# Kernel optimization log

Measured on AMD Instinct MI355X. Metric: run time of the kernel, lower is better.

## Reference

```python
import jax, jax.numpy as jnp
import numpy as np
import math

D = 6       # input_size (raw particle features)
H = 128     # hidden_size
B, N, T = 128, 64, 64  # batch, objects, timesteps (T <= max_len 100)


def setup_inputs() -> dict:
    key = jax.random.key(0)
    ks = jax.random.split(key, 16)
    def lin(k, fan_in, shape):
        return (jax.random.uniform(k, shape, jnp.float32) * 2.0 - 1.0) / np.sqrt(fan_in)
    dm = D + H  # 134, PE / readout feature dim
    return {
        "x": jax.random.normal(ks[0], (B, N, T, D), jnp.float32),
        # particle_embedding Linear(D, H)
        "W_emb": lin(ks[1], D, (D, H)), "b_emb": lin(ks[2], D, (H,)),
        # GRU(H, H): torch layout (3H, in)
        "W_ih": lin(ks[3], H, (3 * H, H)), "W_hh": lin(ks[4], H, (3 * H, H)),
        "b_ih": lin(ks[5], H, (3 * H,)), "b_hh": lin(ks[6], H, (3 * H,)),
        # gate_nn: Linear(dm,H) -> SiLU -> Linear(H,1)
        "Wg1": lin(ks[7], dm, (dm, H)), "bg1": lin(ks[8], dm, (H,)),
        "Wg2": lin(ks[9], H, (H, 1)), "bg2": lin(ks[10], H, (1,)),
        # nn: Linear(dm,H) -> SiLU -> Linear(H,H)
        "Wn1": lin(ks[11], dm, (dm, H)), "bn1": lin(ks[12], dm, (H,)),
        "Wn2": lin(ks[13], H, (H, H)), "bn2": lin(ks[14], H, (H,)),
    }


def _positional_encoding(seq_len, d_model, dtype):
    pos = jnp.arange(seq_len, dtype=dtype)[:, None]                      # [T,1]
    div = jnp.exp(jnp.arange(0, d_model, 2, dtype=dtype) * (-math.log(10000.0) / d_model))
    ang = pos * div                                                       # [T, dm/2]
    # interleave sin (even idx) and cos (odd idx)
    return jnp.stack([jnp.sin(ang), jnp.cos(ang)], axis=-1).reshape(seq_len, d_model)


def _gru_last_hidden(y, W_ih, W_hh, b_ih, b_hh):
    # y: [BN, T, H]; PyTorch GRU gate order: r, z, n
    BN, Tn, Hh = y.shape
    xp = y @ W_ih.T + b_ih                       # [BN, T, 3H], input projections
    def step(h, xp_t):
        gh = h @ W_hh.T + b_hh                   # [BN, 3H]
        xr, xz, xn = jnp.split(xp_t, 3, axis=-1)
        hr, hz, hn = jnp.split(gh, 3, axis=-1)
        r = jax.nn.sigmoid(xr + hr)
        z = jax.nn.sigmoid(xz + hz)
        n = jnp.tanh(xn + r * hn)
        h_new = (1.0 - z) * n + z * h
        return h_new, None
    h0 = jnp.zeros((BN, Hh), y.dtype)
    h_last, _ = jax.lax.scan(step, h0, jnp.swapaxes(xp, 0, 1))
    return h_last                                 # [BN, H]


def reference(x, W_emb, b_emb, W_ih, W_hh, b_ih, b_hh,
              Wg1, bg1, Wg2, bg2, Wn1, bn1, Wn2, bn2):
    Bb, Nn, Tt, Dd = x.shape
    Hh = W_emb.shape[1]
    dm = Dd + Hh
    # particle embedding + GRU over time per (batch, object)
    y = (x @ W_emb + b_emb).reshape(Bb * Nn, Tt, Hh)
    h = _gru_last_hidden(y, W_ih, W_hh, b_ih, b_hh)       # [B*N, H]
    # broadcast last hidden state over timesteps, concat with raw positions
    h_exp = jnp.broadcast_to(h[:, None, :], (Bb * Nn, Tt, Hh))
    aug = jnp.concatenate([x.reshape(Bb * Nn, Tt, Dd), h_exp], axis=-1)  # [B*N, T, dm]
    aug = aug + _positional_encoding(Tt, dm, x.dtype)      # PE (dropout in eval = identity)
    feats = aug.reshape(Bb * Nn * Tt, dm)                  # [M, dm]
    # AttentionalAggregation: segment softmax over batch index
    seg = jnp.repeat(jnp.arange(Bb), Nn * Tt)              # [M]
    gate = jax.nn.silu(feats @ Wg1 + bg1) @ Wg2 + bg2      # [M, 1]
    gate = gate[:, 0]
    val = jax.nn.silu(feats @ Wn1 + bn1) @ Wn2 + bn2       # [M, H]
    gmax = jax.ops.segment_max(gate, seg, num_segments=Bb)
    e = jnp.exp(gate - gmax[seg])
    denom = jax.ops.segment_sum(e, seg, num_segments=Bb)
    w = e / denom[seg]                                      # [M]
    out = jax.ops.segment_sum(w[:, None] * val, seg, num_segments=Bb)  # [B, H]
    return out
```

## Files before the change

### kernel.cpp

```cpp
#include <hip/hip_runtime.h>

using bf8v = __bf16 __attribute__((ext_vector_type(8)));
using s4v  = short  __attribute__((ext_vector_type(4)));
using f4v  = float  __attribute__((ext_vector_type(4)));

#define L2E 1.44269504088896340f

__device__ __forceinline__ float ex2(float x){ float r; asm("v_exp_f32 %0, %1" : "=v"(r) : "v"(x)); return r; }
__device__ __forceinline__ float rcp_(float x){ float r; asm("v_rcp_f32 %0, %1" : "=v"(r) : "v"(x)); return r; }
__device__ __forceinline__ float sigm(float x){ return rcp_(1.0f + ex2(-L2E*x)); }
__device__ __forceinline__ float tanh_(float x){ return 1.0f - 2.0f*rcp_(1.0f + ex2(2.0f*L2E*x)); }
__device__ __forceinline__ short f2bf(float x){ return __builtin_bit_cast(short, (__bf16)x); }
__device__ __forceinline__ f4v splat4(float v){ f4v r = {v,v,v,v}; return r; }
__device__ __forceinline__ f4v mfma16(bf8v a, bf8v b, f4v c){
  return __builtin_amdgcn_mfma_f32_16x16x32_bf16(a, b, c, 0, 0, 0);
}

__global__ void prep_kernel(
    const float* __restrict__ x,
    const float* __restrict__ W_emb, const float* __restrict__ b_emb,
    const float* __restrict__ W_ih,  const float* __restrict__ W_hh,
    const float* __restrict__ b_ih,
    const float* __restrict__ Wg1,   const float* __restrict__ Wn1,
    const float* __restrict__ Wn2,
    const float* __restrict__ bg1,   const float* __restrict__ bn1,
    short* __restrict__ bhhf, short* __restrict__ wcf, short* __restrict__ wn2f,
    short* __restrict__ w2f, float* __restrict__ b2, float* __restrict__ pe,
    float* __restrict__ bc, short* __restrict__ xfrag)
{
  int i = blockIdx.x*256 + threadIdx.x;
  if (i < 49152){
    int e = i&7, lane=(i>>3)&63, r=i>>9; int nt=r%24, kb=r/24;
    int k = kb*32 + ((lane>>4)<<3) + e;
    int n = nt*16 + (lane&15);
    bhhf[i] = f2bf(W_hh[n*128 + k]);
    return;
  }
  i -= 49152;
  if (i < 40960){
    int e=i&7, lane=(i>>3)&63, r=i>>9; int nt=r%16, kb=r/16;
    int k = kb*32 + ((lane>>4)<<3) + e; int n = nt*16 + (lane&15);
    float v = 0.f;
    if (k < 134) v = (n < 128) ? Wg1[k*128 + n] : Wn1[k*128 + (n-128)];
    wcf[i] = f2bf(v);
    return;
  }
  i -= 40960;
  if (i < 16384){
    int e=i&7, lane=(i>>3)&63, r=i>>9; int nt=r%8, kb=r/8;
    int k = kb*32 + ((lane>>4)<<3) + e; int n = nt*16 + (lane&15);
    wn2f[i] = f2bf(Wn2[k*128 + n]);
    return;
  }
  i -= 16384;
  if (i < 12288){
    int e=i&7, lane=(i>>3)&63, nt=i>>9;
    int k = ((lane>>4)<<3) + e; int n = nt*16 + (lane&15);
    float v = 0.f;
    if (k < 6){
      const float* we = W_emb + k*128; const float* wi = W_ih + n*128;
      float s = 0.f;
      for (int h2=0; h2<128; ++h2) s += we[h2]*wi[h2];
      v = s;
    }
    w2f[i] = f2bf(v);
    return;
  }
  i -= 12288;
  if (i < 384){
    float s = b_ih[i]; const float* wi = W_ih + i*128;
    for (int h2=0; h2<128; ++h2) s += b_emb[h2]*wi[h2];
    b2[i] = s;
    return;
  }
  i -= 384;
  if (i < 10240){
    int t = i/160, k = i%160;
    float v = 0.f;
    if (k < 134){
      float fr = expf(-(float)(k & ~1) * 9.210340371976184f / 134.f);
      float a = (float)t * fr;
      v = (k&1) ? cosf(a) : sinf(a);
    }
    pe[i] = v;
    return;
  }
  i -= 10240;
  if (i < 256){ bc[i] = (i < 128) ? bg1[i] : bn1[i-128]; return; }
  i -= 256;
  if (i < 524288){
    int r = i & 15, t = (i>>4)&63, grp = i>>10;
    const float* xr = x + ((size_t)(grp*16 + r)*64 + t)*6;
    s4v lo, hi;
    lo[0]=f2bf(xr[0]); lo[1]=f2bf(xr[1]); lo[2]=f2bf(xr[2]); lo[3]=f2bf(xr[3]);
    hi[0]=f2bf(xr[4]); hi[1]=f2bf(xr[5]); hi[2]=0; hi[3]=0;
    *reinterpret_cast<s4v*>(xfrag + (size_t)i*8)     = lo;
    *reinterpret_cast<s4v*>(xfrag + (size_t)i*8 + 4) = hi;
    return;
  }
}

__global__ __launch_bounds__(512, 2) void gru_kernel(
    const short* __restrict__ xfrag,
    const short* __restrict__ bhhf,
    const short* __restrict__ w2f,
    const float* __restrict__ b2,
    const float* __restrict__ b_hh,
    float* __restrict__ h_out)
{
  __shared__ alignas(16) short h_lds[2][2][16*128];
  const int tid = threadIdx.x;
  const int w = tid >> 6;
  const int lane = tid & 63;
  const int l15 = lane & 15, lhi = lane >> 4;
  const int blk = blockIdx.x;

  for (int i = tid; i < 16*128; i += 512){ h_lds[0][0][i] = 0; h_lds[1][0][i] = 0; }

  bf8v bhh[4][3]; bf8v w2v[3];
  float b2v[3], bhv[3];
  #pragma unroll
  for (int g = 0; g < 3; ++g){
    int nt = g*8 + w;
    w2v[g] = *reinterpret_cast<const bf8v*>(w2f + ((nt*64 + lane)<<3));
    #pragma unroll
    for (int kb = 0; kb < 4; ++kb)
      bhh[kb][g] = *reinterpret_cast<const bf8v*>(bhhf + (((kb*24 + nt)*64 + lane)<<3));
    int col = nt*16 + l15;
    b2v[g] = b2[col]; bhv[g] = b_hh[col];
  }
  float hr0[4] = {0.f,0.f,0.f,0.f};
  float hr1[4] = {0.f,0.f,0.f,0.f};
  __syncthreads();

  const short* xf0 = xfrag + (size_t)(2*blk  )*8192 + l15*8;
  const short* xf1 = xfrag + (size_t)(2*blk+1)*8192 + l15*8;
  const int sw_r = (l15 & 7) << 4;

  bf8v ax0 = *reinterpret_cast<const bf8v*>(xf0);
  bf8v ax1 = *reinterpret_cast<const bf8v*>(xf1);

#define GSTEP(P, T)                                                           \
  {                                                                           \
    int tn = (T) + 1; if (tn > 63) tn = 63;                                   \
    bf8v axn0 = *reinterpret_cast<const bf8v*>(xf0 + tn*128);                 \
    bf8v axn1 = *reinterpret_cast<const bf8v*>(xf1 + tn*128);                 \
    bf8v ah0[4], ah1[4];                                                      \
    _Pragma("unroll")                                                         \
    for (int kb = 0; kb < 4; ++kb){                                           \
      int off = l15*256 + ((kb*64 + lhi*16) ^ sw_r);                          \
      ah0[kb] = *reinterpret_cast<const bf8v*>((const char*)h_lds[0][P] + off); \
      ah1[kb] = *reinterpret_cast<const bf8v*>((const char*)h_lds[1][P] + off); \
    }                                                                         \
    f4v xg0[3], gh0[3], xg1[3], gh1[3];                                       \
    _Pragma("unroll")                                                         \
    for (int g = 0; g < 3; ++g){                                              \
      xg0[g] = splat4(b2v[g]); xg0[g] = mfma16(ax0, w2v[g], xg0[g]);          \
      xg1[g] = splat4(b2v[g]); xg1[g] = mfma16(ax1, w2v[g], xg1[g]);          \
      gh0[g] = splat4(bhv[g]); gh1[g] = splat4(bhv[g]);                       \
      _Pragma("unroll")                                                       \
      for (int kb = 0; kb < 4; ++kb){                                         \
        gh0[g] = mfma16(ah0[kb], bhh[kb][g], gh0[g]);                         \
        gh1[g] = mfma16(ah1[kb], bhh[kb][g], gh1[g]);                         \
      }                                                                       \
    }                                                                         \
    _Pragma("unroll")                                                         \
    for (int r = 0; r < 4; ++r){                                              \
      int s = lhi*4 + r;                                                      \
      int woff = s*256 + (((w*16 + l15)*2) ^ ((s&7)<<4));                     \
      { float rg = sigm(xg0[0][r] + gh0[0][r]);                               \
        float zg = sigm(xg0[1][r] + gh0[1][r]);                               \
        float ng = tanh_(xg0[2][r] + rg*gh0[2][r]);                           \
        float hv = ng + zg*(hr0[r] - ng); hr0[r] = hv;                        \
        *(short*)((char*)h_lds[0][P^1] + woff) = f2bf(hv); }                  \
      { float rg = sigm(xg1[0][r] + gh1[0][r]);                               \
        float zg = sigm(xg1[1][r] + gh1[1][r]);                               \
        float ng = tanh_(xg1[2][r] + rg*gh1[2][r]);                           \
        float hv = ng + zg*(hr1[r] - ng); hr1[r] = hv;                        \
        *(short*)((char*)h_lds[1][P^1] + woff) = f2bf(hv); }                  \
    }                                                                         \
    ax0 = axn0; ax1 = axn1;                                                   \
    __syncthreads();                                                          \
  }

  for (int tt = 0; tt < 32; ++tt){
    GSTEP(0, 2*tt);
    GSTEP(1, 2*tt + 1);
  }
#undef GSTEP

  #pragma unroll
  for (int r = 0; r < 4; ++r){
    int s = lhi*4 + r;
    h_out[(size_t)((2*blk  )*16 + s)*128 + w*16 + l15] = hr0[r];
    h_out[(size_t)((2*blk+1)*16 + s)*128 + w*16 + l15] = hr1[r];
  }
}

__global__ __launch_bounds__(256, 4) void feats_kernel(
    const float* __restrict__ x, const float* __restrict__ h_out,
    const float* __restrict__ pe,
    const short* __restrict__ wcf, const short* __restrict__ wn2f,
    const float* __restrict__ bc, const float* __restrict__ Wg2,
    const float* __restrict__ bg2, const float* __restrict__ bn2,
    float* __restrict__ partials)
{
  __shared__ alignas(16) char AB[64*320];
  __shared__ alignas(16) float hb[160];
  __shared__ float gp[2][64];
  __shared__ float gate_arr[64];

  const int tid = threadIdx.x;
  const int w = tid >> 6;
  const int lane = tid & 63;
  const int l15 = lane & 15, lhi = lane >> 4;
  const int seq = blockIdx.x;

  if (tid < 160) hb[tid] = (tid >= 6 && tid < 134) ? h_out[(size_t)seq*128 + tid - 6] : 0.f;
  __syncthreads();

  {
    int m = tid >> 2, q = tid & 3, k0 = q*40;
    float xr8[8] = {0.f,0.f,0.f,0.f,0.f,0.f,0.f,0.f};
    if (q == 0){
      const float* xr = x + (size_t)(seq*64 + m)*6;
      #pragma unroll
      for (int j = 0; j < 6; ++j) xr8[j] = xr[j];
    }
    const float* per = pe + m*160 + k0;
    const f4v* hb4 = reinterpret_cast<const f4v*>(hb + k0);
    int swm = (m & 3) << 4;
    #pragma unroll
    for (int j = 0; j < 10; ++j){
      f4v v = hb4[j];
      f4v p4 = *reinterpret_cast<const f4v*>(per + 4*j);
      v += p4;
      if (j < 2){
        v[0] += xr8[4*j+0]; v[1] += xr8[4*j+1];
        v[2] += xr8[4*j+2]; v[3] += xr8[4*j+3];
      }
      s4v o;
      #pragma unroll
      for (int c = 0; c < 4; ++c) o[c] = f2bf(v[c]);
      int off = m*320 + (((k0 + 4*j)*2) ^ swm);
      *reinterpret_cast<s4v*>(AB + off) = o;
    }
  }
  __syncthreads();

  const int ntb = w*4;
  float bcv[4];
  #pragma unroll
  for (int i=0;i<4;++i) bcv[i] = bc[(ntb+i)*16 + l15];
  f4v acc[4][4];
  #pragma unroll
  for (int mt=0;mt<4;++mt)
    #pragma unroll
    for (int i=0;i<4;++i) acc[mt][i] = splat4(bcv[i]);
  #pragma unroll
  for (int kb = 0; kb < 5; ++kb){
    bf8v a[4];
    #pragma unroll
    for (int mt=0;mt<4;++mt){
      int row = l15 + 16*mt;
      int off = row*320 + ((kb*64 + lhi*16) ^ ((row&3)<<4));
      a[mt] = *reinterpret_cast<const bf8v*>(AB + off);
    }
    bf8v b[4];
    #pragma unroll
    for (int i=0;i<4;++i)
      b[i] = *reinterpret_cast<const bf8v*>(wcf + (((kb*16 + ntb + i)*64 + lane)<<3));
    #pragma unroll
    for (int mt=0;mt<4;++mt)
      #pragma unroll
      for (int i=0;i<4;++i) acc[mt][i] = mfma16(a[mt], b[i], acc[mt][i]);
  }
  __syncthreads();

  if (w < 2){
    float wg2v[4];
    #pragma unroll
    for (int i=0;i<4;++i) wg2v[i] = Wg2[(ntb+i)*16 + l15];
    #pragma unroll
    for (int mt=0;mt<4;++mt)
      #pragma unroll
      for (int r=0;r<4;++r){
        float p = 0.f;
        #pragma unroll
        for (int i=0;i<4;++i){ float v = acc[mt][i][r]; p += v*sigm(v)*wg2v[i]; }
        p += __shfl_xor(p, 1); p += __shfl_xor(p, 2);
        p += __shfl_xor(p, 4); p += __shfl_xor(p, 8);
        if (l15 == 0) gp[w][mt*16 + lhi*4 + r] = p;
      }
  } else {
    #pragma unroll
    for (int mt=0;mt<4;++mt)
      #pragma unroll
      for (int i=0;i<4;++i)
        #pragma unroll
        for (int r=0;r<4;++r){
          float v = acc[mt][i][r]; float s = v*sigm(v);
          int row = mt*16 + lhi*4 + r;
          int colb = (((w-2)*4 + i)*16 + l15)*2;
          int off = row*256 + (colb ^ ((row&7)<<4));
          *(short*)(AB + off) = f2bf(s);
        }
  }
  __syncthreads();

  if (tid < 64) gate_arr[tid] = bg2[0] + gp[0][tid] + gp[1][tid];

  const int nt2b = w*2;
  float bn2v[2];
  #pragma unroll
  for (int i=0;i<2;++i) bn2v[i] = bn2[(nt2b+i)*16 + l15];
  f4v acc2[4][2];
  #pragma unroll
  for (int mt=0;mt<4;++mt)
    #pragma unroll
    for (int i=0;i<2;++i) acc2[mt][i] = splat4(bn2v[i]);
  #pragma unroll
  for (int kb = 0; kb < 4; ++kb){
    bf8v a2f[4];
    #pragma unroll
    for (int mt=0;mt<4;++mt){
      int row = l15 + 16*mt;
      int off = row*256 + ((kb*64 + lhi*16) ^ ((row&7)<<4));
      a2f[mt] = *reinterpret_cast<const bf8v*>(AB + off);
    }
    bf8v b2f[2];
    #pragma unroll
    for (int i=0;i<2;++i)
      b2f[i] = *reinterpret_cast<const bf8v*>(wn2f + (((kb*8 + nt2b + i)*64 + lane)<<3));
    #pragma unroll
    for (int mt=0;mt<4;++mt)
      #pragma unroll
      for (int i=0;i<2;++i) acc2[mt][i] = mfma16(a2f[mt], b2f[i], acc2[mt][i]);
  }
  __syncthreads();

  float g = gate_arr[lane];
  float M = g;
  #pragma unroll
  for (int d=1; d<64; d<<=1) M = fmaxf(M, __shfl_xor(M, d));
  float e = ex2((g - M)*L2E);
  float sE = e;
  #pragma unroll
  for (int d=1; d<64; d<<=1) sE += __shfl_xor(sE, d);
  float ev0 = 0.f, ev1 = 0.f;
  #pragma unroll
  for (int mt=0;mt<4;++mt)
    #pragma unroll
    for (int r=0;r<4;++r){
      int row = mt*16 + lhi*4 + r;
      float wm = ex2((gate_arr[row] - M)*L2E);
      ev0 += wm*acc2[mt][0][r];
      ev1 += wm*acc2[mt][1][r];
    }
  ev0 += __shfl_xor(ev0, 16); ev0 += __shfl_xor(ev0, 32);
  ev1 += __shfl_xor(ev1, 16); ev1 += __shfl_xor(ev1, 32);

  float* pb = partials + (size_t)seq*130;
  if (tid == 0){ pb[0] = M; pb[1] = sE; }
  if (lane < 16){
    pb[2 + (nt2b+0)*16 + lane] = ev0;
    pb[2 + (nt2b+1)*16 + lane] = ev1;
  }
}

__global__ void combine_kernel(const float* __restrict__ partials, float* __restrict__ out)
{
  int b = blockIdx.x; int j = threadIdx.x;
  const float* pb = partials + (size_t)b*64*130;
  float M = -3.0e38f;
  for (int p = 0; p < 64; ++p) M = fmaxf(M, pb[p*130]);
  float num = 0.f, den = 0.f;
  for (int p = 0; p < 64; ++p){
    float wm = ex2((pb[p*130] - M)*L2E);
    den += wm * pb[p*130 + 1];
    num += wm * pb[p*130 + 2 + j];
  }
  out[b*128 + j] = num / den;
}

extern "C" void kernel_launch(void* const* d_in, const int* in_sizes, int n_in,
                              void* d_out, int out_size, void* d_ws, size_t ws_size,
                              hipStream_t stream) {
  (void)in_sizes; (void)n_in; (void)out_size; (void)ws_size;
  const float* x     = (const float*)d_in[0];
  const float* W_emb = (const float*)d_in[1];
  const float* b_emb = (const float*)d_in[2];
  const float* W_ih  = (const float*)d_in[3];
  const float* W_hh  = (const float*)d_in[4];
  const float* b_ih  = (const float*)d_in[5];
  const float* b_hh  = (const float*)d_in[6];
  const float* Wg1   = (const float*)d_in[7];
  const float* bg1   = (const float*)d_in[8];
  const float* Wg2   = (const float*)d_in[9];
  const float* bg2   = (const float*)d_in[10];
  const float* Wn1   = (const float*)d_in[11];
  const float* bn1   = (const float*)d_in[12];
  const float* Wn2   = (const float*)d_in[13];
  const float* bn2   = (const float*)d_in[14];

  char* p = (char*)d_ws;
  short* bhhf = (short*)p; p += 98304;
  short* wcf  = (short*)p; p += 81920;
  short* wn2f = (short*)p; p += 32768;
  short* w2f  = (short*)p; p += 24576;
  float* b2   = (float*)p; p += 1536;
  float* pe   = (float*)p; p += 40960;
  float* bc   = (float*)p; p += 1024;
  short* xfrag = (short*)p; p += (size_t)524288*8*2;
  float* h_out    = (float*)p; p += (size_t)8192*128*4;
  float* partials = (float*)p; p += (size_t)8192*130*4;

  prep_kernel<<<2555, 256, 0, stream>>>(x, W_emb, b_emb, W_ih, W_hh, b_ih,
                                        Wg1, Wn1, Wn2, bg1, bn1,
                                        bhhf, wcf, wn2f, w2f, b2, pe, bc, xfrag);
  gru_kernel<<<256, 512, 0, stream>>>(xfrag, bhhf, w2f, b2, b_hh, h_out);
  feats_kernel<<<8192, 256, 0, stream>>>(x, h_out, pe, wcf, wn2f, bc, Wg2, bg2, bn2, partials);
  combine_kernel<<<128, 128, 0, stream>>>(partials, (float*)d_out);
}
```

Measured before the change: 193.3 us.

## Factor first readout layer into per-sequence hidden term and per-timestep bias

The first-layer matmul of the gate and value MLPs is split algebraically. The hidden-state part (constant over timesteps) is computed once per sequence at the end of the GRU kernel. The positional-encoding part plus bias is precomputed as a per-timestep bias table. The feats kernel now only runs a K=32 MFMA over the raw x features, with a constant-1 column that injects the per-sequence hidden term. This removes the K=160 matmul and the LDS staging of concatenated features per block, at the cost of extra work in the GRU epilogue, bf16 rounding of the hidden contribution, and a serial 134-term loop per element in prep.

After: 256.2 us. 1.33x slower.

```diff
diff --git a/kernel.cpp b/kernel.cpp
--- a/kernel.cpp
+++ b/kernel.cpp
@@ -24,9 +24,9 @@
     const float* __restrict__ Wg1,   const float* __restrict__ Wn1,
     const float* __restrict__ Wn2,
     const float* __restrict__ bg1,   const float* __restrict__ bn1,
-    short* __restrict__ bhhf, short* __restrict__ wcf, short* __restrict__ wn2f,
-    short* __restrict__ w2f, float* __restrict__ b2, float* __restrict__ pe,
-    float* __restrict__ bc, short* __restrict__ xfrag)
+    short* __restrict__ bhhf, short* __restrict__ wcxf, short* __restrict__ wchf,
+    short* __restrict__ wn2f, short* __restrict__ w2f, float* __restrict__ b2,
+    short* __restrict__ xfrag, float* __restrict__ rowbiasT)
 {
   int i = blockIdx.x*256 + threadIdx.x;
   if (i < 49152){
@@ -37,15 +37,23 @@
     return;
   }
   i -= 49152;
-  if (i < 40960){
-    int e=i&7, lane=(i>>3)&63, r=i>>9; int nt=r%16, kb=r/16;
-    int k = kb*32 + ((lane>>4)<<3) + e; int n = nt*16 + (lane&15);
+  if (i < 8192){
+    int e=i&7, lane=(i>>3)&63, nt=i>>9;
+    int k = ((lane>>4)<<3) + e; int n = nt*16 + (lane&15);
     float v = 0.f;
-    if (k < 134) v = (n < 128) ? Wg1[k*128 + n] : Wn1[k*128 + (n-128)];
-    wcf[i] = f2bf(v);
-    return;
-  }
-  i -= 40960;
+    if (k < 6) v = (n < 128) ? Wg1[k*128 + n] : Wn1[k*128 + (n-128)];
+    wcxf[i] = f2bf(v);
+    return;
+  }
+  i -= 8192;
+  if (i < 32768){
+    int e=i&7, lane=(i>>3)&63, r=i>>9; int nt=r&15, kb=r>>4;
+    int k = 6 + kb*32 + ((lane>>4)<<3) + e; int n = nt*16 + (lane&15);
+    float v = (n < 128) ? Wg1[k*128 + n] : Wn1[k*128 + (n-128)];
+    wchf[i] = f2bf(v);
+    return;
+  }
+  i -= 32768;
   if (i < 16384){
     int e=i&7, lane=(i>>3)&63, r=i>>9; int nt=r%8, kb=r/8;
     int k = kb*32 + ((lane>>4)<<3) + e; int n = nt*16 + (lane&15);
@@ -74,28 +82,28 @@
     return;
   }
   i -= 384;
-  if (i < 10240){
-    int t = i/160, k = i%160;
-    float v = 0.f;
-    if (k < 134){
-      float fr = expf(-(float)(k & ~1) * 9.210340371976184f / 134.f);
-      float a = (float)t * fr;
-      v = (k&1) ? cosf(a) : sinf(a);
-    }
-    pe[i] = v;
-    return;
-  }
-  i -= 10240;
-  if (i < 256){ bc[i] = (i < 128) ? bg1[i] : bn1[i-128]; return; }
-  i -= 256;
   if (i < 524288){
     int r = i & 15, t = (i>>4)&63, grp = i>>10;
     const float* xr = x + ((size_t)(grp*16 + r)*64 + t)*6;
     s4v lo, hi;
     lo[0]=f2bf(xr[0]); lo[1]=f2bf(xr[1]); lo[2]=f2bf(xr[2]); lo[3]=f2bf(xr[3]);
-    hi[0]=f2bf(xr[4]); hi[1]=f2bf(xr[5]); hi[2]=0; hi[3]=0;
+    hi[0]=f2bf(xr[4]); hi[1]=f2bf(xr[5]); hi[2]=f2bf(1.0f); hi[3]=0;
     *reinterpret_cast<s4v*>(xfrag + (size_t)i*8)     = lo;
     *reinterpret_cast<s4v*>(xfrag + (size_t)i*8 + 4) = hi;
+    return;
+  }
+  i -= 524288;
+  if (i < 16384){
+    int n = i >> 6, t = i & 63;
+    float s = (n < 128) ? bg1[n] : bn1[n-128];
+    for (int k = 0; k < 134; ++k){
+      float fr = expf(-(float)(k & ~1) * 9.210340371976184f / 134.f);
+      float a = (float)t * fr;
+      float p = (k & 1) ? cosf(a) : sinf(a);
+      float wv = (n < 128) ? Wg1[k*128 + n] : Wn1[k*128 + (n-128)];
+      s += p * wv;
+    }
+    rowbiasT[i] = s;
     return;
   }
 }
@@ -106,7 +114,8 @@
     const short* __restrict__ w2f,
     const float* __restrict__ b2,
     const float* __restrict__ b_hh,
-    float* __restrict__ h_out)
+    const short* __restrict__ wchf,
+    short* __restrict__ svb)
 {
   __shared__ alignas(16) short h_lds[2][2][16*128];
   const int tid = threadIdx.x;
@@ -190,23 +199,40 @@
 #undef GSTEP
 
   #pragma unroll
-  for (int r = 0; r < 4; ++r){
-    int s = lhi*4 + r;
-    h_out[(size_t)((2*blk  )*16 + s)*128 + w*16 + l15] = hr0[r];
-    h_out[(size_t)((2*blk+1)*16 + s)*128 + w*16 + l15] = hr1[r];
-  }
-}
-
-__global__ __launch_bounds__(256, 4) void feats_kernel(
-    const float* __restrict__ x, const float* __restrict__ h_out,
-    const float* __restrict__ pe,
-    const short* __restrict__ wcf, const short* __restrict__ wn2f,
-    const float* __restrict__ bc, const float* __restrict__ Wg2,
-    const float* __restrict__ bg2, const float* __restrict__ bn2,
+  for (int s = 0; s < 2; ++s){
+    bf8v ah[4];
+    #pragma unroll
+    for (int kb = 0; kb < 4; ++kb){
+      int off = l15*256 + ((kb*64 + lhi*16) ^ sw_r);
+      ah[kb] = *reinterpret_cast<const bf8v*>((const char*)h_lds[s][0] + off);
+    }
+    #pragma unroll
+    for (int j = 0; j < 2; ++j){
+      int nt = w*2 + j;
+      f4v a = {0.f,0.f,0.f,0.f};
+      #pragma unroll
+      for (int kb = 0; kb < 4; ++kb){
+        bf8v wf = *reinterpret_cast<const bf8v*>(wchf + (((kb*16 + nt)*64 + lane)<<3));
+        a = mfma16(ah[kb], wf, a);
+      }
+      #pragma unroll
+      for (int r = 0; r < 4; ++r){
+        int sq = blk*32 + s*16 + lhi*4 + r;
+        svb[(size_t)sq*256 + nt*16 + l15] = f2bf(a[r]);
+      }
+    }
+  }
+}
+
+__global__ __launch_bounds__(256, 2) void feats_kernel(
+    const short* __restrict__ xfrag, const short* __restrict__ svb,
+    const float* __restrict__ rowbiasT,
+    const short* __restrict__ wcxf, const short* __restrict__ wn2f,
+    const float* __restrict__ Wg2, const float* __restrict__ bg2,
+    const float* __restrict__ bn2,
     float* __restrict__ partials)
 {
-  __shared__ alignas(16) char AB[64*320];
-  __shared__ alignas(16) float hb[160];
+  __shared__ alignas(16) short A2[64*128];
   __shared__ float gp[2][64];
   __shared__ float gate_arr[64];
 
@@ -215,99 +241,72 @@
   const int lane = tid & 63;
   const int l15 = lane & 15, lhi = lane >> 4;
   const int seq = blockIdx.x;
-
-  if (tid < 160) hb[tid] = (tid >= 6 && tid < 134) ? h_out[(size_t)seq*128 + tid - 6] : 0.f;
-  __syncthreads();
-
-  {
-    int m = tid >> 2, q = tid & 3, k0 = q*40;
-    float xr8[8] = {0.f,0.f,0.f,0.f,0.f,0.f,0.f,0.f};
-    if (q == 0){
-      const float* xr = x + (size_t)(seq*64 + m)*6;
-      #pragma unroll
-      for (int j = 0; j < 6; ++j) xr8[j] = xr[j];
-    }
-    const float* per = pe + m*160 + k0;
-    const f4v* hb4 = reinterpret_cast<const f4v*>(hb + k0);
-    int swm = (m & 3) << 4;
-    #pragma unroll
-    for (int j = 0; j < 10; ++j){
-      f4v v = hb4[j];
-      f4v p4 = *reinterpret_cast<const f4v*>(per + 4*j);
-      v += p4;
-      if (j < 2){
-        v[0] += xr8[4*j+0]; v[1] += xr8[4*j+1];
-        v[2] += xr8[4*j+2]; v[3] += xr8[4*j+3];
-      }
-      s4v o;
-      #pragma unroll
-      for (int c = 0; c < 4; ++c) o[c] = f2bf(v[c]);
-      int off = m*320 + (((k0 + 4*j)*2) ^ swm);
-      *reinterpret_cast<s4v*>(AB + off) = o;
-    }
-  }
-  __syncthreads();
-
   const int ntb = w*4;
-  float bcv[4];
-  #pragma unroll
-  for (int i=0;i<4;++i) bcv[i] = bc[(ntb+i)*16 + l15];
-  f4v acc[4][4];
+
+  bf8v bx[4];
+  #pragma unroll
+  for (int mt=0;mt<4;++mt){
+    bf8v z;
+    #pragma unroll
+    for (int e=0;e<8;++e) z[e] = (__bf16)0.f;
+    bx[mt] = z;
+  }
+  if (lhi == 0){
+    const short* xp = xfrag + ((size_t)(seq>>4)*1024 + (seq&15))*8;
+    #pragma unroll
+    for (int mt=0;mt<4;++mt)
+      bx[mt] = *reinterpret_cast<const bf8v*>(xp + (size_t)(mt*16 + l15)*128);
+  }
+
+  float gd[4][4];
   #pragma unroll
   for (int mt=0;mt<4;++mt)
     #pragma unroll
-    for (int i=0;i<4;++i) acc[mt][i] = splat4(bcv[i]);
-  #pragma unroll
-  for (int kb = 0; kb < 5; ++kb){
-    bf8v a[4];
+    for (int r=0;r<4;++r) gd[mt][r] = 0.f;
+
+  #pragma unroll
+  for (int i = 0; i < 4; ++i){
+    const int n16 = (ntb+i)*16;
+    bf8v wb = *reinterpret_cast<const bf8v*>(wcxf + (((ntb+i)*64 + lane)<<3));
+    if (lhi == 0)
+      wb[6] = __builtin_bit_cast(__bf16, svb[(size_t)seq*256 + n16 + l15]);
+    f4v acc[4];
     #pragma unroll
     for (int mt=0;mt<4;++mt){
-      int row = l15 + 16*mt;
-      int off = row*320 + ((kb*64 + lhi*16) ^ ((row&3)<<4));
-      a[mt] = *reinterpret_cast<const bf8v*>(AB + off);
-    }
-    bf8v b[4];
-    #pragma unroll
-    for (int i=0;i<4;++i)
-      b[i] = *reinterpret_cast<const bf8v*>(wcf + (((kb*16 + ntb + i)*64 + lane)<<3));
+      acc[mt] = *reinterpret_cast<const f4v*>(rowbiasT + (size_t)(n16+l15)*64 + mt*16 + lhi*4);
+      acc[mt] = mfma16(bx[mt], wb, acc[mt]);
+    }
+    if (w < 2){
+      float wg2s = Wg2[n16 + l15];
+      #pragma unroll
+      for (int mt=0;mt<4;++mt)
+        #pragma unroll
+        for (int r=0;r<4;++r){ float v = acc[mt][r]; gd[mt][r] += v*sigm(v)*wg2s; }
+    } else {
+      #pragma unroll
+      for (int mt=0;mt<4;++mt)
+        #pragma unroll
+        for (int r=0;r<4;++r){
+          float v = acc[mt][r]; float s = v*sigm(v);
+          int row = mt*16 + lhi*4 + r;
+          int colb = (((w-2)*4 + i)*16 + l15)*2;
+          int off = row*256 + (colb ^ ((row&7)<<4));
+          *(short*)((char*)A2 + off) = f2bf(s);
+        }
+    }
+  }
+  if (w < 2){
     #pragma unroll
     for (int mt=0;mt<4;++mt)
       #pragma unroll
-      for (int i=0;i<4;++i) acc[mt][i] = mfma16(a[mt], b[i], acc[mt][i]);
-  }
-  __syncthreads();
-
-  if (w < 2){
-    float wg2v[4];
-    #pragma unroll
-    for (int i=0;i<4;++i) wg2v[i] = Wg2[(ntb+i)*16 + l15];
-    #pragma unroll
-    for (int mt=0;mt<4;++mt)
-      #pragma unroll
       for (int r=0;r<4;++r){
-        float p = 0.f;
-        #pragma unroll
-        for (int i=0;i<4;++i){ float v = acc[mt][i][r]; p += v*sigm(v)*wg2v[i]; }
+        float p = gd[mt][r];
         p += __shfl_xor(p, 1); p += __shfl_xor(p, 2);
         p += __shfl_xor(p, 4); p += __shfl_xor(p, 8);
         if (l15 == 0) gp[w][mt*16 + lhi*4 + r] = p;
       }
-  } else {
-    #pragma unroll
-    for (int mt=0;mt<4;++mt)
-      #pragma unroll
-      for (int i=0;i<4;++i)
-        #pragma unroll
-        for (int r=0;r<4;++r){
-          float v = acc[mt][i][r]; float s = v*sigm(v);
-          int row = mt*16 + lhi*4 + r;
-          int colb = (((w-2)*4 + i)*16 + l15)*2;
-          int off = row*256 + (colb ^ ((row&7)<<4));
-          *(short*)(AB + off) = f2bf(s);
-        }
   }
   __syncthreads();
-
   if (tid < 64) gate_arr[tid] = bg2[0] + gp[0][tid] + gp[1][tid];
 
   const int nt2b = w*2;
@@ -326,16 +325,14 @@
     for (int mt=0;mt<4;++mt){
       int row = l15 + 16*mt;
       int off = row*256 + ((kb*64 + lhi*16) ^ ((row&7)<<4));
-      a2f[mt] = *reinterpret_cast<const bf8v*>(AB + off);
-    }
-    bf8v b2f[2];
-    #pragma unroll
-    for (int i=0;i<2;++i)
-      b2f[i] = *reinterpret_cast<const bf8v*>(wn2f + (((kb*8 + nt2b + i)*64 + lane)<<3));
-    #pragma unroll
-    for (int mt=0;mt<4;++mt)
-      #pragma unroll
-      for (int i=0;i<2;++i) acc2[mt][i] = mfma16(a2f[mt], b2f[i], acc2[mt][i]);
+      a2f[mt] = *reinterpret_cast<const bf8v*>((const char*)A2 + off);
+    }
+    #pragma unroll
+    for (int i=0;i<2;++i){
+      bf8v b2f = *reinterpret_cast<const bf8v*>(wn2f + (((kb*8 + nt2b+i)*64 + lane)<<3));
+      #pragma unroll
+      for (int mt=0;mt<4;++mt) acc2[mt][i] = mfma16(a2f[mt], b2f, acc2[mt][i]);
+    }
   }
   __syncthreads();
 
@@ -404,21 +401,23 @@
   const float* bn2   = (const float*)d_in[14];
 
   char* p = (char*)d_ws;
-  short* bhhf = (short*)p; p += 98304;
-  short* wcf  = (short*)p; p += 81920;
-  short* wn2f = (short*)p; p += 32768;
-  short* w2f  = (short*)p; p += 24576;
-  float* b2   = (float*)p; p += 1536;
-  float* pe   = (float*)p; p += 40960;
-  float* bc   = (float*)p; p += 1024;
-  short* xfrag = (short*)p; p += (size_t)524288*8*2;
-  float* h_out    = (float*)p; p += (size_t)8192*128*4;
+  short* bhhf    = (short*)p; p += 98304;
+  short* wcxf    = (short*)p; p += 16384;
+  short* wchf    = (short*)p; p += 65536;
+  short* wn2f    = (short*)p; p += 32768;
+  short* w2f     = (short*)p; p += 24576;
+  float* b2      = (float*)p; p += 1536;
+  short* xfrag   = (short*)p; p += 8388608;
+  short* svb     = (short*)p; p += 4194304;
+  float* rowbiasT= (float*)p; p += 65536;
   float* partials = (float*)p; p += (size_t)8192*130*4;
 
-  prep_kernel<<<2555, 256, 0, stream>>>(x, W_emb, b_emb, W_ih, W_hh, b_ih,
+  prep_kernel<<<2578, 256, 0, stream>>>(x, W_emb, b_emb, W_ih, W_hh, b_ih,
                                         Wg1, Wn1, Wn2, bg1, bn1,
-                                        bhhf, wcf, wn2f, w2f, b2, pe, bc, xfrag);
-  gru_kernel<<<256, 512, 0, stream>>>(xfrag, bhhf, w2f, b2, b_hh, h_out);
-  feats_kernel<<<8192, 256, 0, stream>>>(x, h_out, pe, wcf, wn2f, bc, Wg2, bg2, bn2, partials);
+                                        bhhf, wcxf, wchf, wn2f, w2f, b2,
+                                        xfrag, rowbiasT);
+  gru_kernel<<<256, 512, 0, stream>>>(xfrag, bhhf, w2f, b2, b_hh, wchf, svb);
+  feats_kernel<<<8192, 256, 0, stream>>>(xfrag, svb, rowbiasT, wcxf, wn2f,
+                                         Wg2, bg2, bn2, partials);
   combine_kernel<<<128, 128, 0, stream>>>(partials, (float*)d_out);
 }
```
